# Performance work log

Measured on AMD Instinct MI355X. Metric: run time of the kernel, lower is better.

The kernel has to match this reference:

```python
import math
import jax, jax.numpy as jnp
import numpy as np

EPS = 1e-5
THETA = 2.0 ** 16


def ln(x):
    # parameter-free LayerNorm over last dim (biased variance, like torch)
    m = jnp.mean(x, axis=-1, keepdims=True)
    v = jnp.mean((x - m) ** 2, axis=-1, keepdims=True)
    return (x - m) / jnp.sqrt(v + EPS)


def get_freqs(n):
    # quantize(arange(n), 2): floor to even so adjacent pairs share a frequency
    t = jnp.floor(jnp.arange(n, dtype=jnp.float32) / 2.0) * 2.0
    return 1.0 / (THETA ** (t / n)) / (2.0 * math.pi)


def rope(cos, sin, v):
    # v: (B, nh, T, N); cos/sin: (T, N) broadcast
    v_rot = jnp.stack((-v[..., 1::2], v[..., ::2]), axis=-1).reshape(v.shape)
    return v * cos + v_rot * sin


def setup_inputs() -> dict:
    key = jax.random.key(0)
    ks = jax.random.split(key, 6)
    B, T, D, nh, N, V = 2, 2048, 256, 4, 4096, 256
    std = 0.02
    return {
        "idx": jax.random.randint(ks[0], (B, T), 0, V, dtype=jnp.int64 if jax.config.jax_enable_x64 else jnp.int32),
        "embed": jax.random.normal(ks[1], (V, D), jnp.float32) * std,
        "encoder": jax.random.normal(ks[2], (nh, D, N), jnp.float32) * std,
        "encoder_v": jax.random.normal(ks[3], (nh, D, N), jnp.float32) * std,
        "decoder": jax.random.normal(ks[4], (nh * N, D), jnp.float32) * std,
        "lm_head": jax.random.normal(ks[5], (D, V), jnp.float32) * std,
    }


def reference(idx, embed, encoder, encoder_v, decoder, lm_head):
    n_layer = 6
    B, T = idx.shape
    nh, D, N = encoder.shape[0], encoder.shape[1], encoder.shape[2]
    dec = decoder.reshape(nh, N, D)

    # RoPE phase tables (t_offset = 0)
    freqs = get_freqs(N)                                   # (N,)
    phases = jnp.arange(T, dtype=jnp.float32)[:, None] * freqs[None, :]
    ph = (phases % 1.0) * (2.0 * math.pi)
    cos, sin = jnp.cos(ph), jnp.sin(ph)                    # (T, N)

    # strictly-lower causal mask (tril, diagonal=-1)
    mask = jnp.tril(jnp.ones((T, T), dtype=bool), k=-1)

    x = ln(jnp.take(embed, idx, axis=0))                   # (B, T, D)

    for _ in range(n_layer):
        x_latent = jnp.einsum("btd,hdn->bhtn", x, encoder)
        x_sparse = jax.nn.relu(x_latent)                   # (B, nh, T, N)

        QR = rope(cos, sin, x_sparse)
        KR = rope(cos, sin, x_sparse)
        scores = jnp.einsum("bhtn,bhsn->bhts", QR, KR)
        scores = jnp.where(mask, scores, 0.0)
        yKV = jnp.einsum("bhts,bsd->bhtd", scores, x)      # V = x broadcast over heads

        yKV = ln(yKV)
        y_sparse = jax.nn.relu(jnp.einsum("bhtd,hdn->bhtn", yKV, encoder_v))
        xy_sparse = x_sparse * y_sparse                    # gated sparse activations
        yMLP = jnp.einsum("bhtn,hnd->btd", xy_sparse, dec)
        x = ln(x + ln(yMLP))

    logits = jnp.einsum("btd,dv->btv", x, lm_head)
    return logits
```

## Files before the change

kernel.cpp:

```cpp
#include <hip/hip_runtime.h>


typedef unsigned short u16;
typedef unsigned int   u32;
typedef __attribute__((ext_vector_type(8))) short bf8;
typedef __attribute__((ext_vector_type(4))) float f4;

#define T_  2048
#define D_  256
#define NH_ 4
#define NN_ 4096
#define NLAYER 6

#define CSA_OFF  ((size_t)0)
#define CSB_OFF  (CSA_OFF  + 262144)
#define ETH_OFF  (CSB_OFF  + 2097152)
#define ETL_OFF  (ETH_OFF  + 8388608)
#define EVH_OFF  (ETL_OFF  + 8388608)
#define EVL_OFF  (EVH_OFF  + 8388608)
#define DTH_OFF  (EVL_OFF  + 8388608)
#define DTL_OFF  (DTH_OFF  + 8388608)
#define LMH_OFF  (DTL_OFF  + 8388608)
#define LML_OFF  (LMH_OFF  + 131072)
#define X_OFF    (LML_OFF  + 131072)
#define XBH_OFF  (X_OFF    + 2097152)
#define XBL_OFF  (XBH_OFF  + 1048576)
#define XBTH_OFF (XBL_OFF  + 1048576)
#define XBTL_OFF (XBTH_OFF + 1048576)
#define QRH_OFF  (XBTL_OFF + 1048576)
#define QRL_OFF  (QRH_OFF  + 67108864)
#define SH_OFF   (QRL_OFF  + 67108864)
#define SL_OFF   (SH_OFF   + 17825792)
#define YKV_OFF  (SL_OFF   + 17825792)
#define YKBH_OFF (YKV_OFF  + 8388608)
#define YKBL_OFF (YKBH_OFF + 4194304)
#define IDX_END  (YKBL_OFF + 4194304)
#define WS_NEED  (IDX_END  + 16384)

__device__ __forceinline__ u16 f2b(float f) {
  u32 u = __builtin_bit_cast(u32, f);
  u32 r = u + 0x7fffu + ((u >> 16) & 1u);
  return (u16)(r >> 16);
}
__device__ __forceinline__ float b2f(u16 h) {
  u32 u = ((u32)h) << 16;
  return __builtin_bit_cast(float, u);
}
__device__ __forceinline__ float wsum(float v) {
#pragma unroll
  for (int o = 32; o; o >>= 1) v += __shfl_xor(v, o, 64);
  return v;
}
__device__ __forceinline__ float2 trig_ct(const float2* csA, const float2* csB, int t, int pp) {
  float2 a = csA[(t >> 7) * 2048 + pp];
  float2 b = csB[(t & 127) * 2048 + pp];
  return make_float2(a.x * b.x - a.y * b.y, a.x * b.y + a.y * b.x);
}
__device__ __forceinline__ void gld16(const u16* g, short* l) {
  __builtin_amdgcn_global_load_lds(
      (const __attribute__((address_space(1))) u32*)g,
      (__attribute__((address_space(3))) u32*)l, 16, 0, 0);
}
__device__ __forceinline__ void stage_t(const u16* g, int lda, short* s, int wid, int lane) {
  int r8 = lane >> 3;
  int c8 = ((lane & 7) ^ r8) * 8;
#pragma unroll
  for (int j = 0; j < 4; ++j) {
    int row = wid * 32 + j * 8;
    gld16(g + (size_t)(row + r8) * lda + c8, s + row * 64);
  }
}
__device__ __forceinline__ void stage_t8(const u16* g, int lda, short* s, int wid, int lane) {
  int r8 = lane >> 3;
  int c8 = ((lane & 7) ^ r8) * 8;
#pragma unroll
  for (int j = 0; j < 2; ++j) {
    int row = wid * 16 + j * 8;
    gld16(g + (size_t)(row + r8) * lda + c8, s + row * 64);
  }
}
__device__ __forceinline__ void mma64x3(const short* AsH, const short* AsL, const short* BsH,
                                        const short* BsL, int wr, int wc, int lane,
                                        f4 acc[4][4]) {
  int r15 = lane & 15, hi = lane >> 4;
  int sw = (r15 & 7) << 3;
#pragma unroll
  for (int kk = 0; kk < 2; ++kk) {
    int ko = (kk * 32 + hi * 8) ^ sw;
    bf8 ah[4], al[4], bh[4], bl[4];
#pragma unroll
    for (int m = 0; m < 4; ++m) {
      int off = (wr * 64 + m * 16 + r15) * 64 + ko;
      ah[m] = *(const bf8*)(AsH + off);
      al[m] = *(const bf8*)(AsL + off);
    }
#pragma unroll
    for (int n = 0; n < 4; ++n) {
      int off = (wc * 64 + n * 16 + r15) * 64 + ko;
      bh[n] = *(const bf8*)(BsH + off);
      bl[n] = *(const bf8*)(BsL + off);
    }
#pragma unroll
    for (int m = 0; m < 4; ++m)
#pragma unroll
      for (int n = 0; n < 4; ++n) {
        acc[m][n] = __builtin_amdgcn_mfma_f32_16x16x32_bf16(ah[m], bh[n], acc[m][n], 0, 0, 0);
        acc[m][n] = __builtin_amdgcn_mfma_f32_16x16x32_bf16(al[m], bh[n], acc[m][n], 0, 0, 0);
        acc[m][n] = __builtin_amdgcn_mfma_f32_16x16x32_bf16(ah[m], bl[n], acc[m][n], 0, 0, 0);
      }
  }
}
__device__ __forceinline__ void mma64x1(const short* AsH, const short* BsH,
                                        int wr, int wc, int lane, f4 acc[4][4]) {
  int r15 = lane & 15, hi = lane >> 4;
  int sw = (r15 & 7) << 3;
#pragma unroll
  for (int kk = 0; kk < 2; ++kk) {
    int ko = (kk * 32 + hi * 8) ^ sw;
    bf8 ah[4], bh[4];
#pragma unroll
    for (int m = 0; m < 4; ++m)
      ah[m] = *(const bf8*)(AsH + (wr * 64 + m * 16 + r15) * 64 + ko);
#pragma unroll
    for (int n = 0; n < 4; ++n)
      bh[n] = *(const bf8*)(BsH + (wc * 64 + n * 16 + r15) * 64 + ko);
#pragma unroll
    for (int m = 0; m < 4; ++m)
#pragma unroll
      for (int n = 0; n < 4; ++n)
        acc[m][n] = __builtin_amdgcn_mfma_f32_16x16x32_bf16(ah[m], bh[n], acc[m][n], 0, 0, 0);
  }
}
__device__ __forceinline__ void acc_zero(f4 acc[4][4]) {
#pragma unroll
  for (int m = 0; m < 4; ++m)
#pragma unroll
    for (int n = 0; n < 4; ++n)
#pragma unroll
      for (int j = 0; j < 4; ++j) acc[m][n][j] = 0.0f;
}
__device__ __forceinline__ void acc_store_f32(float* F, f4 acc[4][4], int wr, int wc, int lane,
                                              bool relu) {
  int r15 = lane & 15, q = lane >> 4;
#pragma unroll
  for (int m = 0; m < 4; ++m)
#pragma unroll
    for (int n = 0; n < 4; ++n)
#pragma unroll
      for (int j = 0; j < 4; ++j) {
        float v = acc[m][n][j];
        if (relu) v = fmaxf(v, 0.0f);
        F[(wr * 64 + m * 16 + q * 4 + j) * 128 + wc * 64 + n * 16 + r15] = v;
      }
}
__device__ __forceinline__ void acc_store_half(float* F, f4 acc[4][4], int pass, int wr, int wc,
                                               int lane, bool relu) {
  if (wr != pass) return;
  int r15 = lane & 15, q = lane >> 4;
#pragma unroll
  for (int m = 0; m < 4; ++m)
#pragma unroll
    for (int n = 0; n < 4; ++n)
#pragma unroll
      for (int j = 0; j < 4; ++j) {
        float v = acc[m][n][j];
        if (relu) v = fmaxf(v, 0.0f);
        F[(m * 16 + q * 4 + j) * 128 + wc * 64 + n * 16 + r15] = v;
      }
}

__global__ __launch_bounds__(256) void k_costab(float2* csA, float2* csB) {
  int id = blockIdx.x * 256 + threadIdx.x;
  int r = id >> 11, p = id & 2047;
  double freq = exp2(-(double)p / 128.0) * 0.15915494309189533577;
  int t = (r < 16) ? (r * 128) : (r - 16);
  double ph = fmod((double)t * freq, 1.0);
  double ang = ph * 6.2831853071795864769;
  float2 v = make_float2((float)cos(ang), (float)sin(ang));
  if (r < 16) csA[r * 2048 + p] = v;
  else        csB[(r - 16) * 2048 + p] = v;
}

__global__ __launch_bounds__(256) void k_tcast2(const float* __restrict__ in,
                                                u16* __restrict__ outH, u16* __restrict__ outL,
                                                int R, int C) {
  __shared__ float tl[32][33];
  size_t bo = (size_t)blockIdx.z * R * C;
  int tx = threadIdx.x, ty = threadIdx.y;
  int c = blockIdx.x * 32 + tx, r0 = blockIdx.y * 32 + ty;
#pragma unroll
  for (int k = 0; k < 32; k += 8) tl[ty + k][tx] = in[bo + (size_t)(r0 + k) * C + c];
  __syncthreads();
  int rr = blockIdx.y * 32 + tx, cc0 = blockIdx.x * 32 + ty;
#pragma unroll
  for (int k = 0; k < 32; k += 8) {
    float v = tl[tx][ty + k];
    u16 h = f2b(v);
    outH[bo + (size_t)(cc0 + k) * R + rr] = h;
    outL[bo + (size_t)(cc0 + k) * R + rr] = f2b(v - b2f(h));
  }
}

__global__ __launch_bounds__(256) void k_ln_embed(const int* __restrict__ idx,
                                                  const float* __restrict__ embed, int b,
                                                  float* __restrict__ x, u16* __restrict__ xbH,
                                                  u16* __restrict__ xbL) {
  int lane = threadIdx.x & 63, wid = threadIdx.x >> 6;
  int r = blockIdx.x * 4 + wid;
  int id = idx[b * T_ + r] & 255;
  float4 v = ((const float4*)(embed + (size_t)id * 256))[lane];
  float m = wsum(v.x + v.y + v.z + v.w) * (1.0f / 256.0f);
  float d0 = v.x - m, d1 = v.y - m, d2 = v.z - m, d3 = v.w - m;
  float var = wsum(d0 * d0 + d1 * d1 + d2 * d2 + d3 * d3) * (1.0f / 256.0f);
  float rs = 1.0f / sqrtf(var + 1e-5f);
  float y0 = d0 * rs, y1 = d1 * rs, y2 = d2 * rs, y3 = d3 * rs;
  ((float4*)(x + (size_t)r * 256))[lane] = make_float4(y0, y1, y2, y3);
  ushort4 oh, ol;
  oh.x = f2b(y0); ol.x = f2b(y0 - b2f(oh.x));
  oh.y = f2b(y1); ol.y = f2b(y1 - b2f(oh.y));
  oh.z = f2b(y2); ol.z = f2b(y2 - b2f(oh.z));
  oh.w = f2b(y3); ol.w = f2b(y3 - b2f(oh.w));
  ((ushort4*)(xbH + (size_t)r * 256))[lane] = oh;
  ((ushort4*)(xbL + (size_t)r * 256))[lane] = ol;
}

__global__ __launch_bounds__(256) void k_xbt(const u16* __restrict__ xbH,
                                             u16* __restrict__ xbTH) {
  int id = blockIdx.x * 256 + threadIdx.x;
  int t = id & 2047, d = id >> 11;
  xbTH[id] = xbH[(size_t)t * 256 + d];
}

#define GEMM_PRE1                                                       \
  __shared__ short sm1[16384];                                          \
  short* T0 = sm1;                                                      \
  short* T1 = sm1 + 8192;                                               \
  float* bounce = (float*)sm1;                                          \
  int tid = threadIdx.x;                                                \
  int lane = tid & 63, wid = tid >> 6;                                  \
  int wr = wid >> 1, wc = wid & 1;                                      \
  f4 acc[4][4];                                                         \
  acc_zero(acc);

#define GEMM_PRE1D                                                      \
  __shared__ short smd1[32768];                                         \
  float* bounce = (float*)smd1;                                         \
  int tid = threadIdx.x;                                                \
  int lane = tid & 63, wid = tid >> 6;                                  \
  int wr = wid >> 1, wc = wid & 1;                                      \
  f4 acc[4][4];                                                         \
  acc_zero(acc);

__global__ __launch_bounds__(256) void k_g1(const u16* __restrict__ xbH,
                                            const u16* __restrict__ etH,
                                            const float2* __restrict__ csA,
                                            const float2* __restrict__ csB,
                                            u16* __restrict__ QRH) {
  GEMM_PRE1
  int it = blockIdx.x, jt = blockIdx.y, h = blockIdx.z;
  size_t ao = (size_t)it * 128 * 256;
  size_t bo = (size_t)h * NN_ * 256 + (size_t)jt * 128 * 256;
  for (int kb = 0; kb < 4; ++kb) {
    stage_t(xbH + ao + kb * 64, 256, T0, wid, lane);
    stage_t(etH + bo + kb * 64, 256, T1, wid, lane);
    __syncthreads();
    mma64x1(T0, T1, wr, wc, lane, acc);
    __syncthreads();
  }
#pragma unroll
  for (int pass = 0; pass < 2; ++pass) {
    acc_store_half(bounce, acc, pass, wr, wc, lane, true);
    __syncthreads();
    for (int w = 0; w < 16; ++w) {
      int e = w * 256 + tid;
      int rrel = e >> 6, p = e & 63;
      float v0 = bounce[rrel * 128 + 2 * p], v1 = bounce[rrel * 128 + 2 * p + 1];
      int t = it * 128 + pass * 64 + rrel, pp = jt * 64 + p;
      float2 c = trig_ct(csA, csB, t, pp);
      float q0 = v0 * c.x - v1 * c.y;
      float q1 = v1 * c.x + v0 * c.y;
      u32 hi = (u32)f2b(q0) | ((u32)f2b(q1) << 16);
      ((u32*)QRH)[(size_t)(h * T_ + t) * 2048 + pp] = hi;
    }
    __syncthreads();
  }
}

__global__ __launch_bounds__(512) void k_g2(const u16* __restrict__ QRH,
                                            u16* __restrict__ SpH) {
  __shared__ short smp[65536];
  float* bounce = (float*)smp;
  int tid = threadIdx.x;
  int lane = tid & 63, wid = tid >> 6;
  int wr = wid >> 2, wc = wid & 3;
  f4 acc[4][6];
#pragma unroll
  for (int m = 0; m < 4; ++m)
#pragma unroll
    for (int n = 0; n < 6; ++n)
#pragma unroll
      for (int j = 0; j < 4; ++j) acc[m][n][j] = 0.0f;
  int orig = blockIdx.x;
  int xcd = orig & 7, sub = orig >> 3;
  int lb = (xcd < 4 ? xcd * 26 : 104 + (xcd - 4) * 25) + sub;
  int h = lb / 51;
  int rem = lb % 51, i = 0;
  while (rem >= (i + 3) / 3) { rem -= (i + 3) / 3; ++i; }
  int j0 = rem * 3, j1 = j0 + 1, j2 = j0 + 2;
  bool has1 = (j1 <= i), has2 = (j2 <= i);
  size_t base = (size_t)h * T_ * NN_;
  size_t ao = base + (size_t)i * 128 * NN_;
  size_t bo0 = base + (size_t)j0 * 128 * NN_;
  size_t bo1 = base + (size_t)j1 * 128 * NN_;
  size_t bo2 = base + (size_t)j2 * 128 * NN_;
  {
    stage_t8(QRH + ao, NN_, smp, wid, lane);
    stage_t8(QRH + bo0, NN_, smp + 8192, wid, lane);
    if (has1) stage_t8(QRH + bo1, NN_, smp + 16384, wid, lane);
    if (has2) stage_t8(QRH + bo2, NN_, smp + 24576, wid, lane);
  }
  int r15 = lane & 15, hi4 = lane >> 4;
  int sw = (r15 & 7) << 3;
  for (int kb = 0; kb < 64; ++kb) {
    short* cur = smp + (kb & 1) * 32768;
    __syncthreads();
    if (kb + 1 < 64) {
      short* nxt = smp + ((kb + 1) & 1) * 32768;
      stage_t8(QRH + ao + (kb + 1) * 64, NN_, nxt, wid, lane);
      stage_t8(QRH + bo0 + (kb + 1) * 64, NN_, nxt + 8192, wid, lane);
      if (has1) stage_t8(QRH + bo1 + (kb + 1) * 64, NN_, nxt + 16384, wid, lane);
      if (has2) stage_t8(QRH + bo2 + (kb + 1) * 64, NN_, nxt + 24576, wid, lane);
    }
#pragma unroll
    for (int kk = 0; kk < 2; ++kk) {
      int ko = (kk * 32 + hi4 * 8) ^ sw;
      bf8 ah[4];
#pragma unroll
      for (int m = 0; m < 4; ++m)
        ah[m] = *(const bf8*)(cur + (wr * 64 + m * 16 + r15) * 64 + ko);
#pragma unroll
      for (int n = 0; n < 6; ++n) {
        int cn = wc * 96 + n * 16;
        int bp = cn >> 7;
        if (bp == 1 && !has1) continue;
        if (bp == 2 && !has2) continue;
        bf8 bh = *(const bf8*)(cur + 8192 + bp * 8192 + ((cn & 127) + r15) * 64 + ko);
#pragma unroll
        for (int m = 0; m < 4; ++m)
          acc[m][n] = __builtin_amdgcn_mfma_f32_16x16x32_bf16(ah[m], bh, acc[m][n], 0, 0, 0);
      }
    }
  }
  __syncthreads();
  int q4 = lane >> 4;
#pragma unroll
  for (int jb = 0; jb < 3; ++jb) {
    if (jb == 1 && !has1) break;
    if (jb == 2 && !has2) break;
    int j = j0 + jb;
    size_t dblk = ((size_t)h * 136 + (size_t)i * (i + 1) / 2 + j) * 16384;
    bool diag = (i == j);
#pragma unroll
    for (int pass = 0; pass < 2; ++pass) {
      if (wr == pass) {
#pragma unroll
        for (int m = 0; m < 4; ++m)
#pragma unroll
          for (int n = 0; n < 6; ++n) {
            int cn = wc * 96 + n * 16;
            if ((cn >> 7) != jb) continue;
#pragma unroll
            for (int jj = 0; jj < 4; ++jj)
              bounce[(m * 16 + q4 * 4 + jj) * 128 + (cn & 127) + r15] = acc[m][n][jj];
          }
      }
      __syncthreads();
      for (int w = 0; w < 8; ++w) {
        int e = w * 512 + tid;
        int rrel = e >> 6, p = e & 63;
        int row = pass * 64 + rrel;
        float s0 = bounce[rrel * 128 + 2 * p], s1 = bounce[rrel * 128 + 2 * p + 1];
        if (diag) {
          if (2 * p >= row) s0 = 0.0f;
          if (2 * p + 1 >= row) s1 = 0.0f;
        }
        u32 hi = (u32)f2b(s0) | ((u32)f2b(s1) << 16);
        ((u32*)SpH)[(dblk >> 1) + row * 64 + p] = hi;
      }
      __syncthreads();
    }
  }
}

__global__ __launch_bounds__(256) void k_g3(const u16* __restrict__ SpH,
                                            const u16* __restrict__ xbTH,
                                            float* __restrict__ yKV0,
                                            float* __restrict__ yKV1) {
  GEMM_PRE1D
  int i = blockIdx.x, jt = blockIdx.y;
  int h = blockIdx.z & 3, ks = blockIdx.z >> 2;
  size_t tri = (size_t)h * 136 + (size_t)i * (i + 1) / 2;
  size_t bo = (size_t)jt * 128 * T_;
  int k0 = ks * (i + 1), k1 = (ks + 1) * (i + 1);
  {
    size_t aoff = (tri + (k0 >> 1)) * 16384 + (k0 & 1) * 64;
    stage_t(SpH + aoff, 128, smd1, wid, lane);
    stage_t(xbTH + bo + k0 * 64, T_, smd1 + 8192, wid, lane);
  }
  for (int kb = k0; kb < k1; ++kb) {
    short* cur = smd1 + ((kb - k0) & 1) * 16384;
    __syncthreads();
    if (kb + 1 < k1) {
      short* nxt = smd1 + ((kb + 1 - k0) & 1) * 16384;
      size_t aoff = (tri + ((kb + 1) >> 1)) * 16384 + ((kb + 1) & 1) * 64;
      stage_t(SpH + aoff, 128, nxt, wid, lane);
      stage_t(xbTH + bo + (kb + 1) * 64, T_, nxt + 8192, wid, lane);
    }
    mma64x1(cur, cur + 8192, wr, wc, lane, acc);
  }
  __syncthreads();
  float* yout = ks ? yKV1 : yKV0;
#pragma unroll
  for (int pass = 0; pass < 2; ++pass) {
    acc_store_half(bounce, acc, pass, wr, wc, lane, false);
    __syncthreads();
    for (int w = 0; w < 32; ++w) {
      int e = w * 256 + tid;
      int row = e >> 7, col = e & 127;
      yout[((size_t)h * T_ + i * 128 + pass * 64 + row) * 256 + jt * 128 + col] =
          bounce[row * 128 + col];
    }
    __syncthreads();
  }
}

__global__ __launch_bounds__(256) void k_ln_f32(const float* __restrict__ in0,
                                                const float* __restrict__ in1,
                                                u16* __restrict__ outH) {
  int lane = threadIdx.x & 63, wid = threadIdx.x >> 6;
  int r = blockIdx.x * 4 + wid;
  float4 a = ((const float4*)(in0 + (size_t)r * 256))[lane];
  float4 b = ((const float4*)(in1 + (size_t)r * 256))[lane];
  float v0 = a.x + b.x, v1 = a.y + b.y, v2 = a.z + b.z, v3 = a.w + b.w;
  float m = wsum(v0 + v1 + v2 + v3) * (1.0f / 256.0f);
  float d0 = v0 - m, d1 = v1 - m, d2 = v2 - m, d3 = v3 - m;
  float var = wsum(d0 * d0 + d1 * d1 + d2 * d2 + d3 * d3) * (1.0f / 256.0f);
  float rs = 1.0f / sqrtf(var + 1e-5f);
  ushort4 oh;
  oh.x = f2b(d0 * rs); oh.y = f2b(d1 * rs); oh.z = f2b(d2 * rs); oh.w = f2b(d3 * rs);
  ((ushort4*)(outH + (size_t)r * 256))[lane] = oh;
}

__global__ __launch_bounds__(256) void k_g4a(const u16* __restrict__ ykH,
                                             const u16* __restrict__ evH,
                                             const float2* __restrict__ csA,
                                             const float2* __restrict__ csB,
                                             u16* __restrict__ QRH) {
  GEMM_PRE1
  int it = blockIdx.x, jt = blockIdx.y, h = blockIdx.z;
  int t0 = it * 128;
  size_t ao = (size_t)(h * T_ + t0) * 256;
  size_t bo = (size_t)h * NN_ * 256 + (size_t)jt * 128 * 256;
  for (int kb = 0; kb < 4; ++kb) {
    stage_t(ykH + ao + kb * 64, 256, T0, wid, lane);
    stage_t(evH + bo + kb * 64, 256, T1, wid, lane);
    __syncthreads();
    mma64x1(T0, T1, wr, wc, lane, acc);
    __syncthreads();
  }
#pragma unroll
  for (int pass = 0; pass < 2; ++pass) {
    acc_store_half(bounce, acc, pass, wr, wc, lane, true);
    __syncthreads();
    for (int w = 0; w < 16; ++w) {
      int e = w * 256 + tid;
      int rrel = e >> 6, p = e & 63;
      float ys0 = bounce[rrel * 128 + 2 * p], ys1 = bounce[rrel * 128 + 2 * p + 1];
      int t = t0 + pass * 64 + rrel, pp = jt * 64 + p;
      size_t u32b = (size_t)(h * T_ + t) * 2048 + pp;
      u32 qh = ((const u32*)QRH)[u32b];
      float qe = b2f((u16)(qh & 0xffff));
      float qo = b2f((u16)(qh >> 16));
      float2 c = trig_ct(csA, csB, t, pp);
      float xe = fmaxf(qe * c.x + qo * c.y, 0.0f);
      float xo = fmaxf(qo * c.x - qe * c.y, 0.0f);
      u32 hi = (u32)f2b(ys0 * xe) | ((u32)f2b(ys1 * xo) << 16);
      ((u32*)QRH)[u32b] = hi;
    }
    __syncthreads();
  }
}

__global__ __launch_bounds__(256) void k_g4b(const u16* __restrict__ xyH,
                                             const u16* __restrict__ dtH,
                                             float* __restrict__ part) {
  GEMM_PRE1D
  int it = blockIdx.x, jt = blockIdx.y;
  int h = blockIdx.z & 3, ks = blockIdx.z >> 2;
  int t0 = it * 128;
  size_t ao = (size_t)(h * T_ + t0) * NN_;
  size_t bo = (size_t)h * D_ * NN_ + (size_t)jt * 128 * NN_;
  int k0 = ks * 32, k1 = ks * 32 + 32;
  {
    stage_t(xyH + ao + k0 * 64, NN_, smd1, wid, lane);
    stage_t(dtH + bo + k0 * 64, NN_, smd1 + 8192, wid, lane);
  }
  for (int kb = k0; kb < k1; ++kb) {
    short* cur = smd1 + ((kb - k0) & 1) * 16384;
    __syncthreads();
    if (kb + 1 < k1) {
      short* nxt = smd1 + ((kb + 1 - k0) & 1) * 16384;
      stage_t(xyH + ao + (kb + 1) * 64, NN_, nxt, wid, lane);
      stage_t(dtH + bo + (kb + 1) * 64, NN_, nxt + 8192, wid, lane);
    }
    mma64x1(cur, cur + 8192, wr, wc, lane, acc);
  }
  __syncthreads();
#pragma unroll
  for (int pass = 0; pass < 2; ++pass) {
    acc_store_half(bounce, acc, pass, wr, wc, lane, false);
    __syncthreads();
    for (int w = 0; w < 32; ++w) {
      int e = w * 256 + tid;
      int row = e >> 7, col = e & 127;
      part[((size_t)blockIdx.z * T_ + t0 + pass * 64 + row) * 256 + jt * 128 + col] =
          bounce[row * 128 + col];
    }
    __syncthreads();
  }
}

__global__ __launch_bounds__(256) void k_ln3(const float* __restrict__ part, float* __restrict__ x,
                                             u16* __restrict__ xbH, u16* __restrict__ xbL) {
  int lane = threadIdx.x & 63, wid = threadIdx.x >> 6;
  int r = blockIdx.x * 4 + wid;
  float a0 = 0, a1 = 0, a2 = 0, a3 = 0;
#pragma unroll
  for (int h = 0; h < 8; ++h) {
    float4 u = ((const float4*)(part + ((size_t)h * T_ + r) * 256))[lane];
    a0 += u.x; a1 += u.y; a2 += u.z; a3 += u.w;
  }
  float m = wsum(a0 + a1 + a2 + a3) * (1.0f / 256.0f);
  float d0 = a0 - m, d1 = a1 - m, d2 = a2 - m, d3 = a3 - m;
  float var = wsum(d0 * d0 + d1 * d1 + d2 * d2 + d3 * d3) * (1.0f / 256.0f);
  float rs = 1.0f / sqrtf(var + 1e-5f);
  float4 xv = ((const float4*)(x + (size_t)r * 256))[lane];
  float s0 = xv.x + d0 * rs, s1 = xv.y + d1 * rs, s2 = xv.z + d2 * rs, s3 = xv.w + d3 * rs;
  float m2 = wsum(s0 + s1 + s2 + s3) * (1.0f / 256.0f);
  float e0 = s0 - m2, e1 = s1 - m2, e2 = s2 - m2, e3 = s3 - m2;
  float var2 = wsum(e0 * e0 + e1 * e1 + e2 * e2 + e3 * e3) * (1.0f / 256.0f);
  float rs2 = 1.0f / sqrtf(var2 + 1e-5f);
  float y0 = e0 * rs2, y1 = e1 * rs2, y2 = e2 * rs2, y3 = e3 * rs2;
  ((float4*)(x + (size_t)r * 256))[lane] = make_float4(y0, y1, y2, y3);
  ushort4 oh, ol;
  oh.x = f2b(y0); ol.x = f2b(y0 - b2f(oh.x));
  oh.y = f2b(y1); ol.y = f2b(y1 - b2f(oh.y));
  oh.z = f2b(y2); ol.z = f2b(y2 - b2f(oh.z));
  oh.w = f2b(y3); ol.w = f2b(y3 - b2f(oh.w));
  ((ushort4*)(xbH + (size_t)r * 256))[lane] = oh;
  ((ushort4*)(xbL + (size_t)r * 256))[lane] = ol;
}

__global__ __launch_bounds__(256) void k_g5(const u16* __restrict__ xbH,
                                            const u16* __restrict__ xbL,
                                            const u16* __restrict__ lmH,
                                            const u16* __restrict__ lmL,
                                            float* __restrict__ out) {
  __shared__ float smf[16384];
  short* AsH = (short*)smf;
  short* AsL = AsH + 8192;
  short* BsH = AsH + 16384;
  short* BsL = AsH + 24576;
  int tid = threadIdx.x;
  int lane = tid & 63, wid = tid >> 6;
  int wr = wid >> 1, wc = wid & 1;
  f4 acc[4][4];
  acc_zero(acc);
  int it = blockIdx.x, jt = blockIdx.y;
  size_t ao = (size_t)it * 128 * 256;
  size_t bo = (size_t)jt * 128 * 256;
  for (int kb = 0; kb < 4; ++kb) {
    stage_t(xbH + ao + kb * 64, 256, AsH, wid, lane);
    stage_t(xbL + ao + kb * 64, 256, AsL, wid, lane);
    stage_t(lmH + bo + kb * 64, 256, BsH, wid, lane);
    stage_t(lmL + bo + kb * 64, 256, BsL, wid, lane);
    __syncthreads();
    mma64x3(AsH, AsL, BsH, BsL, wr, wc, lane, acc);
    __syncthreads();
  }
  acc_store_f32(smf, acc, wr, wc, lane, false);
  __syncthreads();
  for (int w = 0; w < 64; ++w) {
    int e = w * 256 + tid;
    int row = e >> 7, col = e & 127;
    out[(size_t)(it * 128 + row) * 256 + jt * 128 + col] = smf[row * 128 + col];
  }
}

extern "C" void kernel_launch(void* const* d_in, const int* in_sizes, int n_in, void* d_out,
                              int out_size, void* d_ws, size_t ws_size, hipStream_t stream) {
  const int*   idx   = (const int*)d_in[0];
  const float* embed = (const float*)d_in[1];
  const float* enc   = (const float*)d_in[2];
  const float* encv  = (const float*)d_in[3];
  const float* dec   = (const float*)d_in[4];
  const float* lm    = (const float*)d_in[5];

  if (ws_size < WS_NEED) {
    hipMemsetAsync(d_out, 0x46, (size_t)out_size * 4, stream);
    return;
  }

  char* w = (char*)d_ws;
  float2* csA  = (float2*)(w + CSA_OFF);
  float2* csB  = (float2*)(w + CSB_OFF);
  u16*    etH  = (u16*)(w + ETH_OFF);
  u16*    etL  = (u16*)(w + ETL_OFF);
  u16*    evH  = (u16*)(w + EVH_OFF);
  u16*    evL  = (u16*)(w + EVL_OFF);
  u16*    dtH  = (u16*)(w + DTH_OFF);
  u16*    dtL  = (u16*)(w + DTL_OFF);
  u16*    lmH  = (u16*)(w + LMH_OFF);
  u16*    lmL  = (u16*)(w + LML_OFF);
  float*  x    = (float*)(w + X_OFF);
  u16*    xbH  = (u16*)(w + XBH_OFF);
  u16*    xbL  = (u16*)(w + XBL_OFF);
  u16*    xbTH = (u16*)(w + XBTH_OFF);
  u16*    QRH  = (u16*)(w + QRH_OFF);
  u16*    SpH  = (u16*)(w + SH_OFF);
  float*  part = (float*)(w + SH_OFF);
  float*  yKV1 = (float*)(w + SL_OFF);
  float*  yKV0 = (float*)(w + YKV_OFF);
  u16*    ykH  = (u16*)(w + YKBH_OFF);

  k_costab<<<1152, 256, 0, stream>>>(csA, csB);
  k_tcast2<<<dim3(128, 8, 4), dim3(32, 8), 0, stream>>>(enc, etH, etL, 256, 4096);
  k_tcast2<<<dim3(128, 8, 4), dim3(32, 8), 0, stream>>>(encv, evH, evL, 256, 4096);
  k_tcast2<<<dim3(8, 128, 4), dim3(32, 8), 0, stream>>>(dec, dtH, dtL, 4096, 256);
  k_tcast2<<<dim3(8, 8, 1), dim3(32, 8), 0, stream>>>(lm, lmH, lmL, 256, 256);

  for (int b = 0; b < 2; ++b) {
    k_ln_embed<<<512, 256, 0, stream>>>(idx, embed, b, x, xbH, xbL);
    k_xbt<<<2048, 256, 0, stream>>>(xbH, xbTH);
    for (int l = 0; l < NLAYER; ++l) {
      k_g1<<<dim3(16, 32, 4), 256, 0, stream>>>(xbH, etH, csA, csB, QRH);
      k_g2<<<204, 512, 0, stream>>>(QRH, SpH);
      k_g3<<<dim3(16, 2, 8), 256, 0, stream>>>(SpH, xbTH, yKV0, yKV1);
      k_ln_f32<<<2048, 256, 0, stream>>>(yKV0, yKV1, ykH);
      k_g4a<<<dim3(16, 32, 4), 256, 0, stream>>>(ykH, evH, csA, csB, QRH);
      k_g4b<<<dim3(16, 2, 8), 256, 0, stream>>>(QRH, dtH, part);
      k_ln3<<<512, 256, 0, stream>>>(part, x, xbH, xbL);
      k_xbt<<<2048, 256, 0, stream>>>(xbH, xbTH);
    }
    k_g5<<<dim3(16, 2), 256, 0, stream>>>(xbH, xbL, lmH, lmL, (float*)d_out + (size_t)b * T_ * 256);
  }
}
```

Measured before the change: 3.270 ms.

## Batch both sequences into single launches and drop unused low-part weight casts

Instead of looping over the batch on the host, each kernel now processes both batch elements through an extra grid dimension, which doubles the grid size of every launch and halves the number of launches. The k-split in g3 is removed because batching restores occupancy, so each block runs the full causal reduction and the separate partial-sum buffers go away. Encoder, encoder_v and decoder now get a single-output cast kernel that no longer writes the unused low bf16 halves. Workspace buffers double for the batched activations, and g3's longer serial reduction per block may cause load imbalance.

```diff
diff --git a/kernel.cpp b/kernel.cpp
--- a/kernel.cpp
+++ b/kernel.cpp
@@ -12,30 +12,31 @@
 #define NN_ 4096
 #define NLAYER 6
 
+#define XB_E   524288u
+#define QR_E   33554432u
+#define QR_U32 16777216u
+#define SP_U16 8912896u
+#define SP_U32 4456448u
+#define SP_F   4456448u
+#define YKV_F  2097152u
+#define YKH_E  2097152u
+
 #define CSA_OFF  ((size_t)0)
 #define CSB_OFF  (CSA_OFF  + 262144)
 #define ETH_OFF  (CSB_OFF  + 2097152)
-#define ETL_OFF  (ETH_OFF  + 8388608)
-#define EVH_OFF  (ETL_OFF  + 8388608)
-#define EVL_OFF  (EVH_OFF  + 8388608)
-#define DTH_OFF  (EVL_OFF  + 8388608)
-#define DTL_OFF  (DTH_OFF  + 8388608)
-#define LMH_OFF  (DTL_OFF  + 8388608)
+#define EVH_OFF  (ETH_OFF  + 8388608)
+#define DTH_OFF  (EVH_OFF  + 8388608)
+#define LMH_OFF  (DTH_OFF  + 8388608)
 #define LML_OFF  (LMH_OFF  + 131072)
 #define X_OFF    (LML_OFF  + 131072)
-#define XBH_OFF  (X_OFF    + 2097152)
-#define XBL_OFF  (XBH_OFF  + 1048576)
-#define XBTH_OFF (XBL_OFF  + 1048576)
-#define XBTL_OFF (XBTH_OFF + 1048576)
-#define QRH_OFF  (XBTL_OFF + 1048576)
-#define QRL_OFF  (QRH_OFF  + 67108864)
-#define SH_OFF   (QRL_OFF  + 67108864)
-#define SL_OFF   (SH_OFF   + 17825792)
-#define YKV_OFF  (SL_OFF   + 17825792)
-#define YKBH_OFF (YKV_OFF  + 8388608)
-#define YKBL_OFF (YKBH_OFF + 4194304)
-#define IDX_END  (YKBL_OFF + 4194304)
-#define WS_NEED  (IDX_END  + 16384)
+#define XBH_OFF  (X_OFF    + 4194304)
+#define XBL_OFF  (XBH_OFF  + 2097152)
+#define XBTH_OFF (XBL_OFF  + 2097152)
+#define QRH_OFF  (XBTH_OFF + 2097152)
+#define SH_OFF   (QRH_OFF  + 134217728)
+#define YKV_OFF  (SH_OFF   + 35651584)
+#define YKH_OFF  (YKV_OFF  + 16777216)
+#define WS_NEED  (YKH_OFF  + 8388608)
 
 __device__ __forceinline__ u16 f2b(float f) {
   u32 u = __builtin_bit_cast(u32, f);
@@ -181,33 +182,46 @@
   else        csB[(r - 16) * 2048 + p] = v;
 }
 
+__global__ __launch_bounds__(256) void k_tcast1(const float* __restrict__ in,
+                                                u16* __restrict__ outH, int R, int C) {
+  __shared__ float tl[32][33];
+  size_t bo = (size_t)blockIdx.z * R * C;
+  int tx = threadIdx.x, ty = threadIdx.y;
+  int c = blockIdx.x * 32 + tx, r0 = blockIdx.y * 32 + ty;
+#pragma unroll
+  for (int k = 0; k < 32; k += 8) tl[ty + k][tx] = in[bo + (size_t)(r0 + k) * C + c];
+  __syncthreads();
+  int rr = blockIdx.y * 32 + tx, cc0 = blockIdx.x * 32 + ty;
+#pragma unroll
+  for (int k = 0; k < 32; k += 8) outH[bo + (size_t)(cc0 + k) * R + rr] = f2b(tl[tx][ty + k]);
+}
+
 __global__ __launch_bounds__(256) void k_tcast2(const float* __restrict__ in,
                                                 u16* __restrict__ outH, u16* __restrict__ outL,
                                                 int R, int C) {
   __shared__ float tl[32][33];
-  size_t bo = (size_t)blockIdx.z * R * C;
   int tx = threadIdx.x, ty = threadIdx.y;
   int c = blockIdx.x * 32 + tx, r0 = blockIdx.y * 32 + ty;
 #pragma unroll
-  for (int k = 0; k < 32; k += 8) tl[ty + k][tx] = in[bo + (size_t)(r0 + k) * C + c];
+  for (int k = 0; k < 32; k += 8) tl[ty + k][tx] = in[(size_t)(r0 + k) * C + c];
   __syncthreads();
   int rr = blockIdx.y * 32 + tx, cc0 = blockIdx.x * 32 + ty;
 #pragma unroll
   for (int k = 0; k < 32; k += 8) {
     float v = tl[tx][ty + k];
     u16 h = f2b(v);
-    outH[bo + (size_t)(cc0 + k) * R + rr] = h;
-    outL[bo + (size_t)(cc0 + k) * R + rr] = f2b(v - b2f(h));
+    outH[(size_t)(cc0 + k) * R + rr] = h;
+    outL[(size_t)(cc0 + k) * R + rr] = f2b(v - b2f(h));
   }
 }
 
 __global__ __launch_bounds__(256) void k_ln_embed(const int* __restrict__ idx,
-                                                  const float* __restrict__ embed, int b,
+                                                  const float* __restrict__ embed,
                                                   float* __restrict__ x, u16* __restrict__ xbH,
                                                   u16* __restrict__ xbL) {
   int lane = threadIdx.x & 63, wid = threadIdx.x >> 6;
   int r = blockIdx.x * 4 + wid;
-  int id = idx[b * T_ + r] & 255;
+  int id = idx[r] & 255;
   float4 v = ((const float4*)(embed + (size_t)id * 256))[lane];
   float m = wsum(v.x + v.y + v.z + v.w) * (1.0f / 256.0f);
   float d0 = v.x - m, d1 = v.y - m, d2 = v.z - m, d3 = v.w - m;
@@ -227,8 +241,10 @@
 __global__ __launch_bounds__(256) void k_xbt(const u16* __restrict__ xbH,
                                              u16* __restrict__ xbTH) {
   int id = blockIdx.x * 256 + threadIdx.x;
-  int t = id & 2047, d = id >> 11;
-  xbTH[id] = xbH[(size_t)t * 256 + d];
+  int b = id >> 19;
+  int w19 = id & 524287;
+  int t = w19 & 2047, d = w19 >> 11;
+  xbTH[id] = xbH[(size_t)b * XB_E + (size_t)t * 256 + d];
 }
 
 #define GEMM_PRE1                                                       \
@@ -257,8 +273,9 @@
                                             const float2* __restrict__ csB,
                                             u16* __restrict__ QRH) {
   GEMM_PRE1
-  int it = blockIdx.x, jt = blockIdx.y, h = blockIdx.z;
-  size_t ao = (size_t)it * 128 * 256;
+  int it = blockIdx.x, jt = blockIdx.y;
+  int h = blockIdx.z & 3, bb = blockIdx.z >> 2;
+  size_t ao = (size_t)bb * XB_E + (size_t)it * 128 * 256;
   size_t bo = (size_t)h * NN_ * 256 + (size_t)jt * 128 * 256;
   for (int kb = 0; kb < 4; ++kb) {
     stage_t(xbH + ao + kb * 64, 256, T0, wid, lane);
@@ -280,7 +297,7 @@
       float q0 = v0 * c.x - v1 * c.y;
       float q1 = v1 * c.x + v0 * c.y;
       u32 hi = (u32)f2b(q0) | ((u32)f2b(q1) << 16);
-      ((u32*)QRH)[(size_t)(h * T_ + t) * 2048 + pp] = hi;
+      ((u32*)QRH)[(size_t)bb * QR_U32 + (size_t)(h * T_ + t) * 2048 + pp] = hi;
     }
     __syncthreads();
   }
@@ -301,14 +318,15 @@
 #pragma unroll
       for (int j = 0; j < 4; ++j) acc[m][n][j] = 0.0f;
   int orig = blockIdx.x;
-  int xcd = orig & 7, sub = orig >> 3;
-  int lb = (xcd < 4 ? xcd * 26 : 104 + (xcd - 4) * 25) + sub;
-  int h = lb / 51;
-  int rem = lb % 51, i = 0;
+  int lb = (orig & 7) * 51 + (orig >> 3);
+  int bb = lb / 204;
+  int l2 = lb % 204;
+  int h = l2 / 51;
+  int rem = l2 % 51, i = 0;
   while (rem >= (i + 3) / 3) { rem -= (i + 3) / 3; ++i; }
   int j0 = rem * 3, j1 = j0 + 1, j2 = j0 + 2;
   bool has1 = (j1 <= i), has2 = (j2 <= i);
-  size_t base = (size_t)h * T_ * NN_;
+  size_t base = (size_t)bb * QR_E + (size_t)h * T_ * NN_;
   size_t ao = base + (size_t)i * 128 * NN_;
   size_t bo0 = base + (size_t)j0 * 128 * NN_;
   size_t bo1 = base + (size_t)j1 * 128 * NN_;
@@ -385,7 +403,7 @@
           if (2 * p + 1 >= row) s1 = 0.0f;
         }
         u32 hi = (u32)f2b(s0) | ((u32)f2b(s1) << 16);
-        ((u32*)SpH)[(dblk >> 1) + row * 64 + p] = hi;
+        ((u32*)SpH)[(size_t)bb * SP_U32 + (dblk >> 1) + row * 64 + p] = hi;
       }
       __syncthreads();
     }
@@ -394,24 +412,22 @@
 
 __global__ __launch_bounds__(256) void k_g3(const u16* __restrict__ SpH,
                                             const u16* __restrict__ xbTH,
-                                            float* __restrict__ yKV0,
-                                            float* __restrict__ yKV1) {
+                                            float* __restrict__ yKV) {
   GEMM_PRE1D
   int i = blockIdx.x, jt = blockIdx.y;
-  int h = blockIdx.z & 3, ks = blockIdx.z >> 2;
-  size_t tri = (size_t)h * 136 + (size_t)i * (i + 1) / 2;
-  size_t bo = (size_t)jt * 128 * T_;
-  int k0 = ks * (i + 1), k1 = (ks + 1) * (i + 1);
+  int h = blockIdx.z & 3, bb = blockIdx.z >> 2;
+  size_t tri = (size_t)bb * 544 + (size_t)h * 136 + (size_t)i * (i + 1) / 2;
+  size_t bo = (size_t)bb * XB_E + (size_t)jt * 128 * T_;
+  int nk = 2 * (i + 1);
   {
-    size_t aoff = (tri + (k0 >> 1)) * 16384 + (k0 & 1) * 64;
-    stage_t(SpH + aoff, 128, smd1, wid, lane);
-    stage_t(xbTH + bo + k0 * 64, T_, smd1 + 8192, wid, lane);
-  }
-  for (int kb = k0; kb < k1; ++kb) {
-    short* cur = smd1 + ((kb - k0) & 1) * 16384;
-    __syncthreads();
-    if (kb + 1 < k1) {
-      short* nxt = smd1 + ((kb + 1 - k0) & 1) * 16384;
+    stage_t(SpH + tri * 16384, 128, smd1, wid, lane);
+    stage_t(xbTH + bo, T_, smd1 + 8192, wid, lane);
+  }
+  for (int kb = 0; kb < nk; ++kb) {
+    short* cur = smd1 + (kb & 1) * 16384;
+    __syncthreads();
+    if (kb + 1 < nk) {
+      short* nxt = smd1 + ((kb + 1) & 1) * 16384;
       size_t aoff = (tri + ((kb + 1) >> 1)) * 16384 + ((kb + 1) & 1) * 64;
       stage_t(SpH + aoff, 128, nxt, wid, lane);
       stage_t(xbTH + bo + (kb + 1) * 64, T_, nxt + 8192, wid, lane);
@@ -419,7 +435,6 @@
     mma64x1(cur, cur + 8192, wr, wc, lane, acc);
   }
   __syncthreads();
-  float* yout = ks ? yKV1 : yKV0;
 #pragma unroll
   for (int pass = 0; pass < 2; ++pass) {
     acc_store_half(bounce, acc, pass, wr, wc, lane, false);
@@ -427,23 +442,20 @@
     for (int w = 0; w < 32; ++w) {
       int e = w * 256 + tid;
       int row = e >> 7, col = e & 127;
-      yout[((size_t)h * T_ + i * 128 + pass * 64 + row) * 256 + jt * 128 + col] =
+      yKV[(size_t)bb * YKV_F + ((size_t)h * T_ + i * 128 + pass * 64 + row) * 256 + jt * 128 + col] =
           bounce[row * 128 + col];
     }
     __syncthreads();
   }
 }
 
-__global__ __launch_bounds__(256) void k_ln_f32(const float* __restrict__ in0,
-                                                const float* __restrict__ in1,
+__global__ __launch_bounds__(256) void k_ln_f32(const float* __restrict__ in,
                                                 u16* __restrict__ outH) {
   int lane = threadIdx.x & 63, wid = threadIdx.x >> 6;
   int r = blockIdx.x * 4 + wid;
-  float4 a = ((const float4*)(in0 + (size_t)r * 256))[lane];
-  float4 b = ((const float4*)(in1 + (size_t)r * 256))[lane];
-  float v0 = a.x + b.x, v1 = a.y + b.y, v2 = a.z + b.z, v3 = a.w + b.w;
-  float m = wsum(v0 + v1 + v2 + v3) * (1.0f / 256.0f);
-  float d0 = v0 - m, d1 = v1 - m, d2 = v2 - m, d3 = v3 - m;
+  float4 v = ((const float4*)(in + (size_t)r * 256))[lane];
+  float m = wsum(v.x + v.y + v.z + v.w) * (1.0f / 256.0f);
+  float d0 = v.x - m, d1 = v.y - m, d2 = v.z - m, d3 = v.w - m;
   float var = wsum(d0 * d0 + d1 * d1 + d2 * d2 + d3 * d3) * (1.0f / 256.0f);
   float rs = 1.0f / sqrtf(var + 1e-5f);
   ushort4 oh;
@@ -457,9 +469,10 @@
                                              const float2* __restrict__ csB,
                                              u16* __restrict__ QRH) {
   GEMM_PRE1
-  int it = blockIdx.x, jt = blockIdx.y, h = blockIdx.z;
+  int it = blockIdx.x, jt = blockIdx.y;
+  int h = blockIdx.z & 3, bb = blockIdx.z >> 2;
   int t0 = it * 128;
-  size_t ao = (size_t)(h * T_ + t0) * 256;
+  size_t ao = (size_t)bb * YKH_E + (size_t)(h * T_ + t0) * 256;
   size_t bo = (size_t)h * NN_ * 256 + (size_t)jt * 128 * 256;
   for (int kb = 0; kb < 4; ++kb) {
     stage_t(ykH + ao + kb * 64, 256, T0, wid, lane);
@@ -477,7 +490,7 @@
       int rrel = e >> 6, p = e & 63;
       float ys0 = bounce[rrel * 128 + 2 * p], ys1 = bounce[rrel * 128 + 2 * p + 1];
       int t = t0 + pass * 64 + rrel, pp = jt * 64 + p;
-      size_t u32b = (size_t)(h * T_ + t) * 2048 + pp;
+      size_t u32b = (size_t)bb * QR_U32 + (size_t)(h * T_ + t) * 2048 + pp;
       u32 qh = ((const u32*)QRH)[u32b];
       float qe = b2f((u16)(qh & 0xffff));
       float qo = b2f((u16)(qh >> 16));
@@ -496,9 +509,10 @@
                                              float* __restrict__ part) {
   GEMM_PRE1D
   int it = blockIdx.x, jt = blockIdx.y;
-  int h = blockIdx.z & 3, ks = blockIdx.z >> 2;
+  int h = blockIdx.z & 3, ks = (blockIdx.z >> 2) & 1, bb = blockIdx.z >> 3;
+  int z8 = h + 4 * ks;
   int t0 = it * 128;
-  size_t ao = (size_t)(h * T_ + t0) * NN_;
+  size_t ao = (size_t)bb * QR_E + (size_t)(h * T_ + t0) * NN_;
   size_t bo = (size_t)h * D_ * NN_ + (size_t)jt * 128 * NN_;
   int k0 = ks * 32, k1 = ks * 32 + 32;
   {
@@ -523,7 +537,7 @@
     for (int w = 0; w < 32; ++w) {
       int e = w * 256 + tid;
       int row = e >> 7, col = e & 127;
-      part[((size_t)blockIdx.z * T_ + t0 + pass * 64 + row) * 256 + jt * 128 + col] =
+      part[(size_t)bb * SP_F + ((size_t)z8 * T_ + t0 + pass * 64 + row) * 256 + jt * 128 + col] =
           bounce[row * 128 + col];
     }
     __syncthreads();
@@ -534,10 +548,12 @@
                                              u16* __restrict__ xbH, u16* __restrict__ xbL) {
   int lane = threadIdx.x & 63, wid = threadIdx.x >> 6;
   int r = blockIdx.x * 4 + wid;
+  int bb = r >> 11, rl = r & 2047;
+  const float* P = part + (size_t)bb * SP_F;
   float a0 = 0, a1 = 0, a2 = 0, a3 = 0;
 #pragma unroll
   for (int h = 0; h < 8; ++h) {
-    float4 u = ((const float4*)(part + ((size_t)h * T_ + r) * 256))[lane];
+    float4 u = ((const float4*)(P + ((size_t)h * T_ + rl) * 256))[lane];
     a0 += u.x; a1 += u.y; a2 += u.z; a3 += u.w;
   }
   float m = wsum(a0 + a1 + a2 + a3) * (1.0f / 256.0f);
@@ -615,11 +631,8 @@
   float2* csA  = (float2*)(w + CSA_OFF);
   float2* csB  = (float2*)(w + CSB_OFF);
   u16*    etH  = (u16*)(w + ETH_OFF);
-  u16*    etL  = (u16*)(w + ETL_OFF);
   u16*    evH  = (u16*)(w + EVH_OFF);
-  u16*    evL  = (u16*)(w + EVL_OFF);
   u16*    dtH  = (u16*)(w + DTH_OFF);
-  u16*    dtL  = (u16*)(w + DTL_OFF);
   u16*    lmH  = (u16*)(w + LMH_OFF);
   u16*    lmL  = (u16*)(w + LML_OFF);
   float*  x    = (float*)(w + X_OFF);
@@ -629,29 +642,26 @@
   u16*    QRH  = (u16*)(w + QRH_OFF);
   u16*    SpH  = (u16*)(w + SH_OFF);
   float*  part = (float*)(w + SH_OFF);
-  float*  yKV1 = (float*)(w + SL_OFF);
-  float*  yKV0 = (float*)(w + YKV_OFF);
-  u16*    ykH  = (u16*)(w + YKBH_OFF);
+  float*  yKV  = (float*)(w + YKV_OFF);
+  u16*    ykH  = (u16*)(w + YKH_OFF);
 
   k_costab<<<1152, 256, 0, stream>>>(csA, csB);
-  k_tcast2<<<dim3(128, 8, 4), dim3(32, 8), 0, stream>>>(enc, etH, etL, 256, 4096);
-  k_tcast2<<<dim3(128, 8, 4), dim3(32, 8), 0, stream>>>(encv, evH, evL, 256, 4096);
-  k_tcast2<<<dim3(8, 128, 4), dim3(32, 8), 0, stream>>>(dec, dtH, dtL, 4096, 256);
+  k_tcast1<<<dim3(128, 8, 4), dim3(32, 8), 0, stream>>>(enc, etH, 256, 4096);
+  k_tcast1<<<dim3(128, 8, 4), dim3(32, 8), 0, stream>>>(encv, evH, 256, 4096);
+  k_tcast1<<<dim3(8, 128, 4), dim3(32, 8), 0, stream>>>(dec, dtH, 4096, 256);
   k_tcast2<<<dim3(8, 8, 1), dim3(32, 8), 0, stream>>>(lm, lmH, lmL, 256, 256);
-
-  for (int b = 0; b < 2; ++b) {
-    k_ln_embed<<<512, 256, 0, stream>>>(idx, embed, b, x, xbH, xbL);
-    k_xbt<<<2048, 256, 0, stream>>>(xbH, xbTH);
-    for (int l = 0; l < NLAYER; ++l) {
-      k_g1<<<dim3(16, 32, 4), 256, 0, stream>>>(xbH, etH, csA, csB, QRH);
-      k_g2<<<204, 512, 0, stream>>>(QRH, SpH);
-      k_g3<<<dim3(16, 2, 8), 256, 0, stream>>>(SpH, xbTH, yKV0, yKV1);
-      k_ln_f32<<<2048, 256, 0, stream>>>(yKV0, yKV1, ykH);
-      k_g4a<<<dim3(16, 32, 4), 256, 0, stream>>>(ykH, evH, csA, csB, QRH);
-      k_g4b<<<dim3(16, 2, 8), 256, 0, stream>>>(QRH, dtH, part);
-      k_ln3<<<512, 256, 0, stream>>>(part, x, xbH, xbL);
-      k_xbt<<<2048, 256, 0, stream>>>(xbH, xbTH);
-    }
-    k_g5<<<dim3(16, 2), 256, 0, stream>>>(xbH, xbL, lmH, lmL, (float*)d_out + (size_t)b * T_ * 256);
-  }
-}
+  k_ln_embed<<<1024, 256, 0, stream>>>(idx, embed, x, xbH, xbL);
+  k_xbt<<<4096, 256, 0, stream>>>(xbH, xbTH);
+
+  for (int l = 0; l < NLAYER; ++l) {
+    k_g1<<<dim3(16, 32, 8), 256, 0, stream>>>(xbH, etH, csA, csB, QRH);
+    k_g2<<<408, 512, 0, stream>>>(QRH, SpH);
+    k_g3<<<dim3(16, 2, 8), 256, 0, stream>>>(SpH, xbTH, yKV);
+    k_ln_f32<<<4096, 256, 0, stream>>>(yKV, ykH);
+    k_g4a<<<dim3(16, 32, 8), 256, 0, stream>>>(ykH, evH, csA, csB, QRH);
+    k_g4b<<<dim3(16, 2, 16), 256, 0, stream>>>(QRH, dtH, part);
+    k_ln3<<<1024, 256, 0, stream>>>(part, x, xbH, xbL);
+    k_xbt<<<4096, 256, 0, stream>>>(xbH, xbTH);
+  }
+  k_g5<<<dim3(32, 2), 256, 0, stream>>>(xbH, xbL, lmH, lmL, (float*)d_out);
+}
```

Result: faster. 3.022 ms (-7.6%).
